# Optimization experiments

Hardware: AMD Instinct MI355X
Metric: run time of the kernel (lower is better)

## Reference

```python
import jax, jax.numpy as jnp
import numpy as np

B, N, F_IN, F_OUT, H = 4, 2048, 128, 256, 4
HD = F_OUT // H


def setup_inputs() -> dict:
    key = jax.random.key(0)
    k1, k2, k3, k4, k5 = jax.random.split(key, 5)
    x = jax.random.normal(k1, (B, N, F_IN), dtype=jnp.float32)
    adj = jax.random.randint(k2, (B, N, N), 0, 2, dtype=jnp.int32)
    # xavier-ish scaled params
    W = jax.random.normal(k3, (F_OUT, F_IN), dtype=jnp.float32) * float(np.sqrt(2.0 / (F_IN + F_OUT)))
    a_l = jax.random.normal(k4, (H, HD), dtype=jnp.float32) * float(np.sqrt(2.0 / (H * HD + 1)))
    a_r = jax.random.normal(k5, (H, HD), dtype=jnp.float32) * float(np.sqrt(2.0 / (H * HD + 1)))
    return {"x": x, "adj": adj, "W": W, "a_l": a_l, "a_r": a_r}


def reference(x, adj, W, a_l, a_r):
    Bb, Nn, _ = x.shape
    h = jnp.einsum('bnf,of->bno', x, W).reshape(Bb, Nn, H, HD)   # [B,N,H,HD]
    e_l = jnp.einsum('bnhd,hd->bnh', h, a_l)                      # [B,N,H]
    e_r = jnp.einsum('bnhd,hd->bnh', h, a_r)                      # [B,N,H]
    e = e_l[:, :, None, :] + e_r[:, None, :, :]                   # [B,N(i),N(j),H]
    e = jax.nn.leaky_relu(e, negative_slope=0.2)
    e = jnp.where(adj[..., None] == 0, -jnp.inf, e)
    alpha = jax.nn.softmax(e, axis=2)                             # softmax over neighbors j
    out = jnp.einsum('bijh,bjhd->bihd', alpha, h)                 # [B,N,H,HD]
    return out.reshape(Bb, Nn, F_OUT)
```

## Files before the change

### kernel.cpp

```cpp
#include <hip/hip_runtime.h>
#include <stdint.h>

#define BB 4
#define NN 2048
#define F_IN 128
#define F_OUT 256
#define NH 4
#define HD 64

typedef float f32x4 __attribute__((ext_vector_type(4)));
typedef float f32x2 __attribute__((ext_vector_type(2)));
typedef short s16x8 __attribute__((ext_vector_type(8)));
typedef int i32x4 __attribute__((ext_vector_type(4)));
typedef unsigned long long u64;
typedef unsigned short u16;

#define LOG2E 1.4426950408889634f

__device__ __forceinline__ u16 f32_to_bf16_rtn(float f) {
    union { float f; uint32_t u; } v; v.f = f;
    uint32_t u = v.u;
    u += 0x7fffu + ((u >> 16) & 1u);
    return (u16)(u >> 16);
}

__device__ __forceinline__ float exp2_fast(float x) {
#if __has_builtin(__builtin_amdgcn_exp2f)
    return __builtin_amdgcn_exp2f(x);
#else
    return exp2f(x);
#endif
}

__device__ __forceinline__ int sbfe1(uint32_t v, int k) {
#if __has_builtin(__builtin_amdgcn_sbfe)
    return __builtin_amdgcn_sbfe((int)v, k, 1);
#else
    return ((int32_t)(v << (31 - k))) >> 31;
#endif
}

__global__ __launch_bounds__(256) void k01(
    const int* __restrict__ adj, const float* __restrict__ x,
    const float* __restrict__ W, const float* __restrict__ a_l,
    const float* __restrict__ a_r, u64* __restrict__ abits,
    u16* __restrict__ hB, float* __restrict__ el, f32x2* __restrict__ er12)
{
    const int t = threadIdx.x;

    __shared__ __align__(16) float red[4 * 64 * 20];
    float (*xs)[F_IN] = (float(*)[F_IN])red;

    if (blockIdx.x >= 512) {
        const int wid = ((blockIdx.x - 512) << 2) | (t >> 6);
        const int lane = t & 63;
        const int* rowp = adj + (size_t)wid * NN;
        u64 mym = 0;
        for (int g = 0; g < 4; ++g) {
            int v[8];
#pragma unroll
            for (int u = 0; u < 8; ++u)
                v[u] = __builtin_nontemporal_load(rowp + (g * 8 + u) * 64 + lane);
#pragma unroll
            for (int u = 0; u < 8; ++u) {
                u64 m = __ballot(v[u] != 0);
                if (lane == g * 8 + u) mym = m;
            }
        }
        if (lane < 32) abits[(size_t)wid * 32 + lane] = mym;
        return;
    }

    const int b = blockIdx.x >> 7;
    const int n0 = (blockIdx.x & 127) * 16;

    {
        const f32x4* src = (const f32x4*)(x + ((size_t)b * NN + n0) * F_IN);
        f32x4* dst = (f32x4*)&xs[0][0];
        dst[t] = src[t];
        dst[t + 256] = src[t + 256];
    }
    __syncthreads();

    float acc[16];
#pragma unroll
    for (int n = 0; n < 16; ++n) acc[n] = 0.f;

    const float* wrow = W + (size_t)t * F_IN;
#pragma unroll 2
    for (int k0 = 0; k0 < F_IN; k0 += 8) {
        f32x4 w0 = *(const f32x4*)(wrow + k0);
        f32x4 w1 = *(const f32x4*)(wrow + k0 + 4);
#pragma unroll
        for (int n = 0; n < 16; ++n) {
            f32x4 xa = *(const f32x4*)&xs[n][k0];
            f32x4 xb = *(const f32x4*)&xs[n][k0 + 4];
            float s = acc[n];
            s = fmaf(xa[0], w0[0], s); s = fmaf(xa[1], w0[1], s);
            s = fmaf(xa[2], w0[2], s); s = fmaf(xa[3], w0[3], s);
            s = fmaf(xb[0], w1[0], s); s = fmaf(xb[1], w1[1], s);
            s = fmaf(xb[2], w1[2], s); s = fmaf(xb[3], w1[3], s);
            acc[n] = s;
        }
    }
    __syncthreads();

    const int w = t >> 6, lane = t & 63;
    const float al = a_l[t];
    const float ar = a_r[t];
    const int n_ = lane & 15, og = lane >> 4;
    float sl, sr;
    {
        float* rp = &red[((size_t)w * 64 + lane) * 20];
#pragma unroll
        for (int q = 0; q < 4; ++q) {
            f32x4 v;
#pragma unroll
            for (int e = 0; e < 4; ++e) v[e] = acc[q * 4 + e] * al;
            *(f32x4*)(rp + q * 4) = v;
        }
    }
    __syncthreads();
    {
        float s = 0.f;
#pragma unroll
        for (int oo = 0; oo < 16; ++oo)
            s += red[((size_t)w * 64 + og + 4 * oo) * 20 + n_];
        s += __shfl_xor(s, 16, 64); s += __shfl_xor(s, 32, 64);
        sl = s;
    }
    __syncthreads();
    {
        float* rp = &red[((size_t)w * 64 + lane) * 20];
#pragma unroll
        for (int q = 0; q < 4; ++q) {
            f32x4 v;
#pragma unroll
            for (int e = 0; e < 4; ++e) v[e] = acc[q * 4 + e] * ar;
            *(f32x4*)(rp + q * 4) = v;
        }
    }
    __syncthreads();
    {
        float s = 0.f;
#pragma unroll
        for (int oo = 0; oo < 16; ++oo)
            s += red[((size_t)w * 64 + og + 4 * oo) * 20 + n_];
        s += __shfl_xor(s, 16, 64); s += __shfl_xor(s, 32, 64);
        sr = s;
    }
    if (lane < 16) {
        el[((size_t)b * NH + w) * NN + n0 + lane] = sl * LOG2E;
        float sre = sr * LOG2E;
        f32x2 v2; v2[0] = exp2_fast(sre); v2[1] = exp2_fast(0.2f * sre);
        er12[((size_t)b * NH + w) * NN + n0 + lane] = v2;
    }

    const int dcol = t & 15, cb = (t >> 4) & 3;
    const int jt32 = n0 >> 5;
    const int lb = dcol + ((n0 >> 3) & 2) * 16;
    u16* hb = hB + ((((size_t)b * 64 + jt32) * 4 + w) * 4 + cb) * 512 + (size_t)lb * 8;
    s16x8 pk0, pk1;
#pragma unroll
    for (int n = 0; n < 8; ++n) pk0[n] = (short)f32_to_bf16_rtn(acc[n]);
#pragma unroll
    for (int n = 0; n < 8; ++n) pk1[n] = (short)f32_to_bf16_rtn(acc[n + 8]);
    *(s16x8*)hb         = pk0;
    *(s16x8*)(hb + 128) = pk1;
}

#define MSTRIDE 68

__global__ __launch_bounds__(256, 3) void k2_attn(
    const uint32_t* __restrict__ abits32, const u16* __restrict__ hB,
    const float* __restrict__ el, const f32x2* __restrict__ er12,
    float* __restrict__ out)
{
    __shared__ __align__(16) char smem[33792];
    float*    er_lds   = (float*)smem;
    uint32_t* mask_lds = (uint32_t*)(smem + 16384);
    float*    racc     = (float*)smem;

    const int t = threadIdx.x;
    const int jq = t >> 6, l = t & 63;
    const int o = blockIdx.x;
    const int kblk = o >> 3;
    const int bw = (o & 7) + 8 * (kblk & 1);
    const int b = bw >> 2;
    const int w = bw & 3;
    const int i0 = (kblk >> 1) * 32;
    const int r = l & 15;
    const int kb = l >> 4;
    const int ks = kb * 8;
    const int irow0 = i0 + r, irow1 = irow0 + 16;

    {
        const f32x4* gsrc = (const f32x4*)(er12 + (size_t)(b * NH + w) * NN);
        f32x4* edst = (f32x4*)er_lds;
#pragma unroll
        for (int p = 0; p < 4; ++p) edst[t + p * 256] = gsrc[t + p * 256];
        const i32x4* msrc = (const i32x4*)(abits32 + ((size_t)b * NN + i0) * 64);
        i32x4 mv0 = msrc[t * 2];
        i32x4 mv1 = msrc[t * 2 + 1];
        const int mrow = t >> 3, mc = (t & 7) * 8;
        *(i32x4*)&mask_lds[mrow * MSTRIDE + mc]     = mv0;
        *(i32x4*)&mask_lds[mrow * MSTRIDE + mc + 4] = mv1;
    }

    const u16* hbp = hB + ((((size_t)b * 64 + jq * 16) * 4 + w) * 4) * 512 + (size_t)l * 8;
    const float eli0 = el[((size_t)b * NH + w) * NN + irow0];
    const float eli1 = el[((size_t)b * NH + w) * NN + irow1];
    const float E1i0 = exp2_fast(eli0), E2i0 = exp2_fast(0.2f * eli0);
    const float E1i1 = exp2_fast(eli1), E2i1 = exp2_fast(0.2f * eli1);

    f32x4 a00 = {0.f,0.f,0.f,0.f}, a01 = a00, a02 = a00, a03 = a00, as0 = a00;
    f32x4 a10 = a00, a11 = a00, a12 = a00, a13 = a00, as1 = a00;
    s16x8 ones;
#pragma unroll
    for (int k = 0; k < 8; ++k) ones[k] = (short)0x3F80;

    s16x8 b0c = *(const s16x8*)(hbp + 0 * 512);
    s16x8 b1c = *(const s16x8*)(hbp + 1 * 512);
    s16x8 b2c = *(const s16x8*)(hbp + 2 * 512);
    s16x8 b3c = *(const s16x8*)(hbp + 3 * 512);
    __syncthreads();

#define MFMA_BF16 __builtin_amdgcn_mfma_f32_16x16x32_bf16
#define BODY(IT, PF)                                                          \
    {                                                                         \
        const int itv = (IT);                                                 \
        const int jb2 = (jq * 512 + itv * 32 + ks) * 2;                       \
        f32x4 e0 = *(const f32x4*)(er_lds + jb2);                             \
        f32x4 e1 = *(const f32x4*)(er_lds + jb2 + 4);                         \
        f32x4 e2 = *(const f32x4*)(er_lds + jb2 + 8);                         \
        f32x4 e3 = *(const f32x4*)(er_lds + jb2 + 12);                        \
        uint32_t w2a = mask_lds[r * MSTRIDE + jq * 16 + itv] >> ks;           \
        uint32_t w2b = mask_lds[(16 + r) * MSTRIDE + jq * 16 + itv] >> ks;    \
        s16x8 b0n, b1n, b2n, b3n;                                             \
        if (PF) {                                                             \
            const u16* hp_ = hbp + (size_t)(itv + 1) * 8192;                  \
            b0n = *(const s16x8*)(hp_ + 0 * 512);                             \
            b1n = *(const s16x8*)(hp_ + 1 * 512);                             \
            b2n = *(const s16x8*)(hp_ + 2 * 512);                             \
            b3n = *(const s16x8*)(hp_ + 3 * 512);                             \
        }                                                                     \
        __builtin_amdgcn_sched_barrier(0);                                    \
        union { s16x8 v; uint32_t u[4]; } afa, afb;                           \
        _Pragma("unroll")                                                     \
        for (int kk = 0; kk < 4; ++kk) {                                      \
            f32x4 ev = (kk == 0) ? e0 : ((kk == 1) ? e1 : ((kk == 2) ? e2 : e3)); \
            float t00 = E1i0 * ev[0], m00 = E2i0 * ev[1];                     \
            float t01 = E1i0 * ev[2], m01 = E2i0 * ev[3];                     \
            float t10 = E1i1 * ev[0], m10 = E2i1 * ev[1];                     \
            float t11 = E1i1 * ev[2], m11 = E2i1 * ev[3];                     \
            float p00 = fmaxf(t00, m00);           \
            float p01 = fmaxf(t01, m01);                                      \
            float p10 = fmaxf(t10, m10);                                      \
            float p11 = fmaxf(t11, m11);                                      \
            union { float f; uint32_t u; } c00, c01, c10, c11;                \
            c00.f = p00; c01.f = p01; c10.f = p10; c11.f = p11;               \
            uint32_t q00 = c00.u & (uint32_t)sbfe1(w2a, 2 * kk);              \
            uint32_t q01 = c01.u & (uint32_t)sbfe1(w2a, 2 * kk + 1);          \
            uint32_t q10 = c10.u & (uint32_t)sbfe1(w2b, 2 * kk);              \
            uint32_t q11 = c11.u & (uint32_t)sbfe1(w2b, 2 * kk + 1);          \
            afa.u[kk] = __builtin_amdgcn_perm(q01, q00, 0x07060302);          \
            afb.u[kk] = __builtin_amdgcn_perm(q11, q10, 0x07060302);          \
        }                                                                     \
        a00 = MFMA_BF16(afa.v, b0c, a00, 0, 0, 0);                            \
        a01 = MFMA_BF16(afa.v, b1c, a01, 0, 0, 0);                            \
        a02 = MFMA_BF16(afa.v, b2c, a02, 0, 0, 0);                            \
        a03 = MFMA_BF16(afa.v, b3c, a03, 0, 0, 0);                            \
        as0 = MFMA_BF16(afa.v, ones, as0, 0, 0, 0);                           \
        a10 = MFMA_BF16(afb.v, b0c, a10, 0, 0, 0);                            \
        a11 = MFMA_BF16(afb.v, b1c, a11, 0, 0, 0);                            \
        a12 = MFMA_BF16(afb.v, b2c, a12, 0, 0, 0);                            \
        a13 = MFMA_BF16(afb.v, b3c, a13, 0, 0, 0);                            \
        as1 = MFMA_BF16(afb.v, ones, as1, 0, 0, 0);                           \
        if (PF) { b0c = b0n; b1c = b1n; b2c = b2n; b3c = b3n; }               \
    }

    for (int g = 0; g < 3; ++g) {
#pragma unroll
        for (int s = 0; s < 4; ++s) BODY(g * 4 + s, 1);
    }
    BODY(12, 1); BODY(13, 1); BODY(14, 1); BODY(15, 0);

    __syncthreads();
    if (jq > 0) {
        float* p = &racc[((jq - 1) * 64 + l) * 44];
        *(f32x4*)(p +  0) = a00; *(f32x4*)(p +  4) = a01;
        *(f32x4*)(p +  8) = a02; *(f32x4*)(p + 12) = a03;
        *(f32x4*)(p + 16) = as0;
        *(f32x4*)(p + 20) = a10; *(f32x4*)(p + 24) = a11;
        *(f32x4*)(p + 28) = a12; *(f32x4*)(p + 32) = a13;
        *(f32x4*)(p + 36) = as1;
    }
    __syncthreads();
    if (jq == 0) {
#pragma unroll
        for (int s = 0; s < 3; ++s) {
            const float* p = &racc[(s * 64 + l) * 44];
            a00 += *(const f32x4*)(p +  0); a01 += *(const f32x4*)(p +  4);
            a02 += *(const f32x4*)(p +  8); a03 += *(const f32x4*)(p + 12);
            as0 += *(const f32x4*)(p + 16);
            a10 += *(const f32x4*)(p + 20); a11 += *(const f32x4*)(p + 24);
            a12 += *(const f32x4*)(p + 28); a13 += *(const f32x4*)(p + 32);
            as1 += *(const f32x4*)(p + 36);
        }

        float* op = out + ((size_t)b * NN + i0) * F_OUT + w * HD;
#pragma unroll
        for (int q = 0; q < 4; ++q) {
            const int row0 = kb * 4 + q;
            float inv0 = 1.0f / as0[q];
            __builtin_nontemporal_store(a00[q] * inv0, &op[(size_t)row0 * F_OUT +  0 + r]);
            __builtin_nontemporal_store(a01[q] * inv0, &op[(size_t)row0 * F_OUT + 16 + r]);
            __builtin_nontemporal_store(a02[q] * inv0, &op[(size_t)row0 * F_OUT + 32 + r]);
            __builtin_nontemporal_store(a03[q] * inv0, &op[(size_t)row0 * F_OUT + 48 + r]);
            const int row1 = 16 + kb * 4 + q;
            float inv1 = 1.0f / as1[q];
            __builtin_nontemporal_store(a10[q] * inv1, &op[(size_t)row1 * F_OUT +  0 + r]);
            __builtin_nontemporal_store(a11[q] * inv1, &op[(size_t)row1 * F_OUT + 16 + r]);
            __builtin_nontemporal_store(a12[q] * inv1, &op[(size_t)row1 * F_OUT + 32 + r]);
            __builtin_nontemporal_store(a13[q] * inv1, &op[(size_t)row1 * F_OUT + 48 + r]);
        }
    }
}

extern "C" void kernel_launch(void* const* d_in, const int* in_sizes, int n_in,
                              void* d_out, int out_size, void* d_ws, size_t ws_size,
                              hipStream_t stream) {
    const float* x   = (const float*)d_in[0];
    const int*   adj = (const int*)d_in[1];
    const float* W   = (const float*)d_in[2];
    const float* a_l = (const float*)d_in[3];
    const float* a_r = (const float*)d_in[4];
    float* out = (float*)d_out;

    char* ws = (char*)d_ws;
    u16*   hB    = (u16*)ws;
    u64*   abits = (u64*)(ws + (size_t)BB * F_OUT * NN * 2);
    float* el    = (float*)(ws + (size_t)BB * F_OUT * NN * 2 + (size_t)BB * NN * 32 * 8);
    f32x2* er12  = (f32x2*)(el + (size_t)BB * NH * NN);

    k01<<<512 + BB * NN / 4, 256, 0, stream>>>(adj, x, W, a_l, a_r, abits, hB, el, er12);
    k2_attn<<<BB * NH * (NN / 32), 256, 0, stream>>>((const uint32_t*)abits, hB, el, er12, out);
}
```

Baseline: 46.19 us.

## Double attention row tile to 64 and interleave pack/projection blocks in k01

Each attention block now processes 64 query rows instead of 32, so every loaded hB fragment and er vector feeds twice as many MFMAs. This halves the grid and halves redundant reads of h and er. In exchange the kernel uses more LDS (about 63KB) and more accumulator registers, so occupancy drops from 3 to 2 blocks per CU. Separately, k01 interleaves its projection blocks with its adjacency bit-packing blocks (one projection per five blocks) so the two kinds of work overlap on the GPU instead of running in separate phases.

Measured after the change: 56.17 us. 21.6% more time.

```diff
diff --git a/kernel.cpp b/kernel.cpp
--- a/kernel.cpp
+++ b/kernel.cpp
@@ -51,8 +51,10 @@
     __shared__ __align__(16) float red[4 * 64 * 20];
     float (*xs)[F_IN] = (float(*)[F_IN])red;
 
-    if (blockIdx.x >= 512) {
-        const int wid = ((blockIdx.x - 512) << 2) | (t >> 6);
+    const int bid = blockIdx.x;
+    if ((bid % 5) != 4) {
+        const int pack_id = bid - (bid + 1) / 5;
+        const int wid = (pack_id << 2) | (t >> 6);
         const int lane = t & 63;
         const int* rowp = adj + (size_t)wid * NN;
         u64 mym = 0;
@@ -71,8 +73,9 @@
         return;
     }
 
-    const int b = blockIdx.x >> 7;
-    const int n0 = (blockIdx.x & 127) * 16;
+    const int proj_id = bid / 5;
+    const int b = proj_id >> 7;
+    const int n0 = (proj_id & 127) * 16;
 
     {
         const f32x4* src = (const f32x4*)(x + ((size_t)b * NN + n0) * F_IN);
@@ -171,12 +174,12 @@
 
 #define MSTRIDE 68
 
-__global__ __launch_bounds__(256, 3) void k2_attn(
+__global__ __launch_bounds__(256, 2) void k2_attn(
     const uint32_t* __restrict__ abits32, const u16* __restrict__ hB,
     const float* __restrict__ el, const f32x2* __restrict__ er12,
     float* __restrict__ out)
 {
-    __shared__ __align__(16) char smem[33792];
+    __shared__ __align__(16) char smem[64512];
     float*    er_lds   = (float*)smem;
     uint32_t* mask_lds = (uint32_t*)(smem + 16384);
     float*    racc     = (float*)smem;
@@ -188,11 +191,10 @@
     const int bw = (o & 7) + 8 * (kblk & 1);
     const int b = bw >> 2;
     const int w = bw & 3;
-    const int i0 = (kblk >> 1) * 32;
+    const int i0 = (kblk >> 1) * 64;
     const int r = l & 15;
     const int kb = l >> 4;
     const int ks = kb * 8;
-    const int irow0 = i0 + r, irow1 = irow0 + 16;
 
     {
         const f32x4* gsrc = (const f32x4*)(er12 + (size_t)(b * NH + w) * NN);
@@ -200,21 +202,26 @@
 #pragma unroll
         for (int p = 0; p < 4; ++p) edst[t + p * 256] = gsrc[t + p * 256];
         const i32x4* msrc = (const i32x4*)(abits32 + ((size_t)b * NN + i0) * 64);
-        i32x4 mv0 = msrc[t * 2];
-        i32x4 mv1 = msrc[t * 2 + 1];
-        const int mrow = t >> 3, mc = (t & 7) * 8;
-        *(i32x4*)&mask_lds[mrow * MSTRIDE + mc]     = mv0;
-        *(i32x4*)&mask_lds[mrow * MSTRIDE + mc + 4] = mv1;
+#pragma unroll
+        for (int p = 0; p < 4; ++p) {
+            const int vi = p * 256 + t;
+            i32x4 mv = msrc[vi];
+            *(i32x4*)&mask_lds[(vi >> 4) * MSTRIDE + (vi & 15) * 4] = mv;
+        }
     }
 
     const u16* hbp = hB + ((((size_t)b * 64 + jq * 16) * 4 + w) * 4) * 512 + (size_t)l * 8;
-    const float eli0 = el[((size_t)b * NH + w) * NN + irow0];
-    const float eli1 = el[((size_t)b * NH + w) * NN + irow1];
-    const float E1i0 = exp2_fast(eli0), E2i0 = exp2_fast(0.2f * eli0);
-    const float E1i1 = exp2_fast(eli1), E2i1 = exp2_fast(0.2f * eli1);
+    const float* elp = el + ((size_t)b * NH + w) * NN + i0 + r;
+    const float eli0 = elp[0], eli1 = elp[16], eli2 = elp[32], eli3 = elp[48];
+    const float E1a = exp2_fast(eli0), E2a = exp2_fast(0.2f * eli0);
+    const float E1b = exp2_fast(eli1), E2b = exp2_fast(0.2f * eli1);
+    const float E1c = exp2_fast(eli2), E2c = exp2_fast(0.2f * eli2);
+    const float E1d = exp2_fast(eli3), E2d = exp2_fast(0.2f * eli3);
 
     f32x4 a00 = {0.f,0.f,0.f,0.f}, a01 = a00, a02 = a00, a03 = a00, as0 = a00;
     f32x4 a10 = a00, a11 = a00, a12 = a00, a13 = a00, as1 = a00;
+    f32x4 a20 = a00, a21 = a00, a22 = a00, a23 = a00, as2 = a00;
+    f32x4 a30 = a00, a31 = a00, a32 = a00, a33 = a00, as3 = a00;
     s16x8 ones;
 #pragma unroll
     for (int k = 0; k < 8; ++k) ones[k] = (short)0x3F80;
@@ -226,6 +233,18 @@
     __syncthreads();
 
 #define MFMA_BF16 __builtin_amdgcn_mfma_f32_16x16x32_bf16
+#define PGEN(EV, J2, E1, E2, W2, OUTU)                                        \
+    {                                                                         \
+        float t0_ = (E1) * (EV)[0], m0_ = (E2) * (EV)[1];                     \
+        float t1_ = (E1) * (EV)[2], m1_ = (E2) * (EV)[3];                     \
+        float p0_ = fmaxf(t0_, m0_);                                          \
+        float p1_ = fmaxf(t1_, m1_);                                          \
+        union { float f; uint32_t u; } c0_, c1_; c0_.f = p0_; c1_.f = p1_;    \
+        uint32_t q0_ = c0_.u & (uint32_t)sbfe1((W2), 2 * (J2));               \
+        uint32_t q1_ = c1_.u & (uint32_t)sbfe1((W2), 2 * (J2) + 1);           \
+        OUTU = __builtin_amdgcn_perm(q1_, q0_, 0x07060302);                   \
+    }
+
 #define BODY(IT, PF)                                                          \
     {                                                                         \
         const int itv = (IT);                                                 \
@@ -234,8 +253,11 @@
         f32x4 e1 = *(const f32x4*)(er_lds + jb2 + 4);                         \
         f32x4 e2 = *(const f32x4*)(er_lds + jb2 + 8);                         \
         f32x4 e3 = *(const f32x4*)(er_lds + jb2 + 12);                        \
-        uint32_t w2a = mask_lds[r * MSTRIDE + jq * 16 + itv] >> ks;           \
-        uint32_t w2b = mask_lds[(16 + r) * MSTRIDE + jq * 16 + itv] >> ks;    \
+        const int mcol = jq * 16 + itv;                                       \
+        uint32_t w2a = mask_lds[r * MSTRIDE + mcol] >> ks;                    \
+        uint32_t w2b = mask_lds[(16 + r) * MSTRIDE + mcol] >> ks;             \
+        uint32_t w2c = mask_lds[(32 + r) * MSTRIDE + mcol] >> ks;             \
+        uint32_t w2d = mask_lds[(48 + r) * MSTRIDE + mcol] >> ks;             \
         s16x8 b0n, b1n, b2n, b3n;                                             \
         if (PF) {                                                             \
             const u16* hp_ = hbp + (size_t)(itv + 1) * 8192;                  \
@@ -245,26 +267,14 @@
             b3n = *(const s16x8*)(hp_ + 3 * 512);                             \
         }                                                                     \
         __builtin_amdgcn_sched_barrier(0);                                    \
-        union { s16x8 v; uint32_t u[4]; } afa, afb;                           \
+        union { s16x8 v; uint32_t u[4]; } afa, afb, afc, afd;                 \
         _Pragma("unroll")                                                     \
         for (int kk = 0; kk < 4; ++kk) {                                      \
             f32x4 ev = (kk == 0) ? e0 : ((kk == 1) ? e1 : ((kk == 2) ? e2 : e3)); \
-            float t00 = E1i0 * ev[0], m00 = E2i0 * ev[1];                     \
-            float t01 = E1i0 * ev[2], m01 = E2i0 * ev[3];                     \
-            float t10 = E1i1 * ev[0], m10 = E2i1 * ev[1];                     \
-            float t11 = E1i1 * ev[2], m11 = E2i1 * ev[3];                     \
-            float p00 = fmaxf(t00, m00);           \
-            float p01 = fmaxf(t01, m01);                                      \
-            float p10 = fmaxf(t10, m10);                                      \
-            float p11 = fmaxf(t11, m11);                                      \
-            union { float f; uint32_t u; } c00, c01, c10, c11;                \
-            c00.f = p00; c01.f = p01; c10.f = p10; c11.f = p11;               \
-            uint32_t q00 = c00.u & (uint32_t)sbfe1(w2a, 2 * kk);              \
-            uint32_t q01 = c01.u & (uint32_t)sbfe1(w2a, 2 * kk + 1);          \
-            uint32_t q10 = c10.u & (uint32_t)sbfe1(w2b, 2 * kk);              \
-            uint32_t q11 = c11.u & (uint32_t)sbfe1(w2b, 2 * kk + 1);          \
-            afa.u[kk] = __builtin_amdgcn_perm(q01, q00, 0x07060302);          \
-            afb.u[kk] = __builtin_amdgcn_perm(q11, q10, 0x07060302);          \
+            PGEN(ev, kk, E1a, E2a, w2a, afa.u[kk]);                           \
+            PGEN(ev, kk, E1b, E2b, w2b, afb.u[kk]);                           \
+            PGEN(ev, kk, E1c, E2c, w2c, afc.u[kk]);                           \
+            PGEN(ev, kk, E1d, E2d, w2d, afd.u[kk]);                           \
         }                                                                     \
         a00 = MFMA_BF16(afa.v, b0c, a00, 0, 0, 0);                            \
         a01 = MFMA_BF16(afa.v, b1c, a01, 0, 0, 0);                            \
@@ -276,6 +286,16 @@
         a12 = MFMA_BF16(afb.v, b2c, a12, 0, 0, 0);                            \
         a13 = MFMA_BF16(afb.v, b3c, a13, 0, 0, 0);                            \
         as1 = MFMA_BF16(afb.v, ones, as1, 0, 0, 0);                           \
+        a20 = MFMA_BF16(afc.v, b0c, a20, 0, 0, 0);                            \
+        a21 = MFMA_BF16(afc.v, b1c, a21, 0, 0, 0);                            \
+        a22 = MFMA_BF16(afc.v, b2c, a22, 0, 0, 0);                            \
+        a23 = MFMA_BF16(afc.v, b3c, a23, 0, 0, 0);                            \
+        as2 = MFMA_BF16(afc.v, ones, as2, 0, 0, 0);                           \
+        a30 = MFMA_BF16(afd.v, b0c, a30, 0, 0, 0);                            \
+        a31 = MFMA_BF16(afd.v, b1c, a31, 0, 0, 0);                            \
+        a32 = MFMA_BF16(afd.v, b2c, a32, 0, 0, 0);                            \
+        a33 = MFMA_BF16(afd.v, b3c, a33, 0, 0, 0);                            \
+        as3 = MFMA_BF16(afd.v, ones, as3, 0, 0, 0);                           \
         if (PF) { b0c = b0n; b1c = b1n; b2c = b2n; b3c = b3n; }               \
     }
 
@@ -287,42 +307,49 @@
 
     __syncthreads();
     if (jq > 0) {
-        float* p = &racc[((jq - 1) * 64 + l) * 44];
-        *(f32x4*)(p +  0) = a00; *(f32x4*)(p +  4) = a01;
-        *(f32x4*)(p +  8) = a02; *(f32x4*)(p + 12) = a03;
-        *(f32x4*)(p + 16) = as0;
-        *(f32x4*)(p + 20) = a10; *(f32x4*)(p + 24) = a11;
-        *(f32x4*)(p + 28) = a12; *(f32x4*)(p + 32) = a13;
-        *(f32x4*)(p + 36) = as1;
+        float* p = &racc[((jq - 1) * 64 + l) * 84];
+#define STW(OFF, V) *(f32x4*)(p + (OFF)) = V
+        STW(0,a00); STW(4,a01); STW(8,a02); STW(12,a03); STW(16,as0);
+        STW(20,a10); STW(24,a11); STW(28,a12); STW(32,a13); STW(36,as1);
+        STW(40,a20); STW(44,a21); STW(48,a22); STW(52,a23); STW(56,as2);
+        STW(60,a30); STW(64,a31); STW(68,a32); STW(72,a33); STW(76,as3);
+#undef STW
     }
     __syncthreads();
     if (jq == 0) {
 #pragma unroll
         for (int s = 0; s < 3; ++s) {
-            const float* p = &racc[(s * 64 + l) * 44];
-            a00 += *(const f32x4*)(p +  0); a01 += *(const f32x4*)(p +  4);
-            a02 += *(const f32x4*)(p +  8); a03 += *(const f32x4*)(p + 12);
-            as0 += *(const f32x4*)(p + 16);
-            a10 += *(const f32x4*)(p + 20); a11 += *(const f32x4*)(p + 24);
-            a12 += *(const f32x4*)(p + 28); a13 += *(const f32x4*)(p + 32);
-            as1 += *(const f32x4*)(p + 36);
+            const float* p = &racc[(s * 64 + l) * 84];
+#define LDW(OFF, V) V += *(const f32x4*)(p + (OFF))
+            LDW(0,a00); LDW(4,a01); LDW(8,a02); LDW(12,a03); LDW(16,as0);
+            LDW(20,a10); LDW(24,a11); LDW(28,a12); LDW(32,a13); LDW(36,as1);
+            LDW(40,a20); LDW(44,a21); LDW(48,a22); LDW(52,a23); LDW(56,as2);
+            LDW(60,a30); LDW(64,a31); LDW(68,a32); LDW(72,a33); LDW(76,as3);
+#undef LDW
         }
 
         float* op = out + ((size_t)b * NN + i0) * F_OUT + w * HD;
 #pragma unroll
         for (int q = 0; q < 4; ++q) {
-            const int row0 = kb * 4 + q;
-            float inv0 = 1.0f / as0[q];
-            __builtin_nontemporal_store(a00[q] * inv0, &op[(size_t)row0 * F_OUT +  0 + r]);
-            __builtin_nontemporal_store(a01[q] * inv0, &op[(size_t)row0 * F_OUT + 16 + r]);
-            __builtin_nontemporal_store(a02[q] * inv0, &op[(size_t)row0 * F_OUT + 32 + r]);
-            __builtin_nontemporal_store(a03[q] * inv0, &op[(size_t)row0 * F_OUT + 48 + r]);
-            const int row1 = 16 + kb * 4 + q;
-            float inv1 = 1.0f / as1[q];
-            __builtin_nontemporal_store(a10[q] * inv1, &op[(size_t)row1 * F_OUT +  0 + r]);
-            __builtin_nontemporal_store(a11[q] * inv1, &op[(size_t)row1 * F_OUT + 16 + r]);
-            __builtin_nontemporal_store(a12[q] * inv1, &op[(size_t)row1 * F_OUT + 32 + r]);
-            __builtin_nontemporal_store(a13[q] * inv1, &op[(size_t)row1 * F_OUT + 48 + r]);
+            const int rw = kb * 4 + q;
+            float i0v = 1.0f / as0[q], i1v = 1.0f / as1[q];
+            float i2v = 1.0f / as2[q], i3v = 1.0f / as3[q];
+            __builtin_nontemporal_store(a00[q]*i0v, &op[(size_t)(rw    )*F_OUT +  0 + r]);
+            __builtin_nontemporal_store(a01[q]*i0v, &op[(size_t)(rw    )*F_OUT + 16 + r]);
+            __builtin_nontemporal_store(a02[q]*i0v, &op[(size_t)(rw    )*F_OUT + 32 + r]);
+            __builtin_nontemporal_store(a03[q]*i0v, &op[(size_t)(rw    )*F_OUT + 48 + r]);
+            __builtin_nontemporal_store(a10[q]*i1v, &op[(size_t)(rw+16 )*F_OUT +  0 + r]);
+            __builtin_nontemporal_store(a11[q]*i1v, &op[(size_t)(rw+16 )*F_OUT + 16 + r]);
+            __builtin_nontemporal_store(a12[q]*i1v, &op[(size_t)(rw+16 )*F_OUT + 32 + r]);
+            __builtin_nontemporal_store(a13[q]*i1v, &op[(size_t)(rw+16 )*F_OUT + 48 + r]);
+            __builtin_nontemporal_store(a20[q]*i2v, &op[(size_t)(rw+32 )*F_OUT +  0 + r]);
+            __builtin_nontemporal_store(a21[q]*i2v, &op[(size_t)(rw+32 )*F_OUT + 16 + r]);
+            __builtin_nontemporal_store(a22[q]*i2v, &op[(size_t)(rw+32 )*F_OUT + 32 + r]);
+            __builtin_nontemporal_store(a23[q]*i2v, &op[(size_t)(rw+32 )*F_OUT + 48 + r]);
+            __builtin_nontemporal_store(a30[q]*i3v, &op[(size_t)(rw+48 )*F_OUT +  0 + r]);
+            __builtin_nontemporal_store(a31[q]*i3v, &op[(size_t)(rw+48 )*F_OUT + 16 + r]);
+            __builtin_nontemporal_store(a32[q]*i3v, &op[(size_t)(rw+48 )*F_OUT + 32 + r]);
+            __builtin_nontemporal_store(a33[q]*i3v, &op[(size_t)(rw+48 )*F_OUT + 48 + r]);
         }
     }
 }
@@ -343,6 +370,6 @@
     float* el    = (float*)(ws + (size_t)BB * F_OUT * NN * 2 + (size_t)BB * NN * 32 * 8);
     f32x2* er12  = (f32x2*)(el + (size_t)BB * NH * NN);
 
-    k01<<<512 + BB * NN / 4, 256, 0, stream>>>(adj, x, W, a_l, a_r, abits, hB, el, er12);
-    k2_attn<<<BB * NH * (NN / 32), 256, 0, stream>>>((const uint32_t*)abits, hB, el, er12, out);
-}
+    k01<<<2560, 256, 0, stream>>>(adj, x, W, a_l, a_r, abits, hB, el, er12);
+    k2_attn<<<BB * NH * (NN / 64), 256, 0, stream>>>((const uint32_t*)abits, hB, el, er12, out);
+}
```

## Pack adjacency per thread with vector loads and interleave projection blocks

Applied to the files above, without the earlier changes.

Adjacency bit-packing changes from a wave-wide ballot over coalesced scalar loads to each thread reading 32 contiguous ints with 128-bit loads and building one 32-bit mask word. The bit layout in the workspace stays the same. Projection blocks are now interleaved with packing blocks (one in every five), so the compute-heavy projection can overlap with the memory-bound adjacency scan instead of all running at the start of the grid. The per-instruction access pattern is strided, 128 bytes per lane, and the nontemporal hints are dropped, which may hurt DRAM or cache efficiency.

After: 56.10 us. +21.4%, slower.

```diff
diff --git a/kernel.cpp b/kernel.cpp
--- a/kernel.cpp
+++ b/kernel.cpp
@@ -43,7 +43,7 @@
 __global__ __launch_bounds__(256) void k01(
     const int* __restrict__ adj, const float* __restrict__ x,
     const float* __restrict__ W, const float* __restrict__ a_l,
-    const float* __restrict__ a_r, u64* __restrict__ abits,
+    const float* __restrict__ a_r, uint32_t* __restrict__ abits32,
     u16* __restrict__ hB, float* __restrict__ el, f32x2* __restrict__ er12)
 {
     const int t = threadIdx.x;
@@ -51,28 +51,29 @@
     __shared__ __align__(16) float red[4 * 64 * 20];
     float (*xs)[F_IN] = (float(*)[F_IN])red;
 
-    if (blockIdx.x >= 512) {
-        const int wid = ((blockIdx.x - 512) << 2) | (t >> 6);
-        const int lane = t & 63;
-        const int* rowp = adj + (size_t)wid * NN;
-        u64 mym = 0;
-        for (int g = 0; g < 4; ++g) {
-            int v[8];
-#pragma unroll
-            for (int u = 0; u < 8; ++u)
-                v[u] = __builtin_nontemporal_load(rowp + (g * 8 + u) * 64 + lane);
-#pragma unroll
-            for (int u = 0; u < 8; ++u) {
-                u64 m = __ballot(v[u] != 0);
-                if (lane == g * 8 + u) mym = m;
-            }
-        }
-        if (lane < 32) abits[(size_t)wid * 32 + lane] = mym;
+    const int bid = blockIdx.x;
+    if ((bid % 5) != 4) {
+        const int pack_id = bid - (bid + 1) / 5;
+        const int row = (pack_id << 2) | (t >> 6);
+        const int wd = t & 63;
+        const int* wp = adj + (size_t)row * NN + wd * 32;
+        i32x4 v[8];
+#pragma unroll
+        for (int u = 0; u < 8; ++u) v[u] = *(const i32x4*)(wp + 4 * u);
+        uint32_t word = 0;
+#pragma unroll
+        for (int u = 0; u < 8; ++u) {
+#pragma unroll
+            for (int e = 0; e < 4; ++e)
+                word |= (uint32_t)(v[u][e] != 0) << (4 * u + e);
+        }
+        abits32[(size_t)row * 64 + wd] = word;
         return;
     }
 
-    const int b = blockIdx.x >> 7;
-    const int n0 = (blockIdx.x & 127) * 16;
+    const int proj_id = bid / 5;
+    const int b = proj_id >> 7;
+    const int n0 = (proj_id & 127) * 16;
 
     {
         const f32x4* src = (const f32x4*)(x + ((size_t)b * NN + n0) * F_IN);
@@ -338,11 +339,11 @@
     float* out = (float*)d_out;
 
     char* ws = (char*)d_ws;
-    u16*   hB    = (u16*)ws;
-    u64*   abits = (u64*)(ws + (size_t)BB * F_OUT * NN * 2);
-    float* el    = (float*)(ws + (size_t)BB * F_OUT * NN * 2 + (size_t)BB * NN * 32 * 8);
-    f32x2* er12  = (f32x2*)(el + (size_t)BB * NH * NN);
-
-    k01<<<512 + BB * NN / 4, 256, 0, stream>>>(adj, x, W, a_l, a_r, abits, hB, el, er12);
-    k2_attn<<<BB * NH * (NN / 32), 256, 0, stream>>>((const uint32_t*)abits, hB, el, er12, out);
-}
+    u16*      hB      = (u16*)ws;
+    uint32_t* abits32 = (uint32_t*)(ws + (size_t)BB * F_OUT * NN * 2);
+    float*    el      = (float*)(ws + (size_t)BB * F_OUT * NN * 2 + (size_t)BB * NN * 256);
+    f32x2*    er12    = (f32x2*)(el + (size_t)BB * NH * NN);
+
+    k01<<<2560, 256, 0, stream>>>(adj, x, W, a_l, a_r, abits32, hB, el, er12);
+    k2_attn<<<BB * NH * (NN / 32), 256, 0, stream>>>(abits32, hB, el, er12, out);
+}
```
